# Kernel optimization log

Measured on AMD Instinct MI355X. Metric: run time of the kernel, lower is better.

The kernel has to match this reference:

```python
import jax, jax.numpy as jnp
import numpy as np

B, H, S, Q = 32768, 896, 448, 256  # batch, hidden, split=hidden//2, quantisation


def setup_inputs() -> dict:
    key = jax.random.key(0)
    ks = jax.random.split(key, 16)
    sc = 0.02
    return {
        'prev_y': jax.random.uniform(ks[0], (B, 2), jnp.float32) * 2.0 - 1.0,
        'prev_hidden': jax.random.normal(ks[1], (B, H), jnp.float32),
        'current_coarse': jax.random.uniform(ks[2], (B, 1), jnp.float32) * 2.0 - 1.0,
        'W_R': jax.random.normal(ks[3], (H, 3 * H), jnp.float32) * sc,
        'W_Ic': jax.random.normal(ks[4], (2, 3 * S), jnp.float32) * sc,
        'W_If': jax.random.normal(ks[5], (3, 3 * S), jnp.float32) * sc,
        'W_O1': jax.random.normal(ks[6], (S, S), jnp.float32) * sc,
        'b_O1': jnp.zeros((S,), jnp.float32),
        'W_O2': jax.random.normal(ks[7], (S, Q), jnp.float32) * sc,
        'b_O2': jnp.zeros((Q,), jnp.float32),
        'W_O3': jax.random.normal(ks[8], (S, S), jnp.float32) * sc,
        'b_O3': jnp.zeros((S,), jnp.float32),
        'W_O4': jax.random.normal(ks[9], (S, Q), jnp.float32) * sc,
        'b_O4': jnp.zeros((Q,), jnp.float32),
        'bias_u': jnp.zeros((H,), jnp.float32),
        'bias_r': jnp.zeros((H,), jnp.float32),
        'bias_e': jnp.zeros((H,), jnp.float32),
    }


def reference(prev_y, prev_hidden, current_coarse, W_R, W_Ic, W_If,
              W_O1, b_O1, W_O2, b_O2, W_O3, b_O3, W_O4, b_O4,
              bias_u, bias_r, bias_e):
    # recurrent projection of previous hidden state: [B, 3H]
    R_u, R_r, R_e = jnp.split(prev_hidden @ W_R, 3, axis=1)
    # coarse-half input projection from (prev_coarse, prev_fine): [B, 3S]
    I_cu, I_cr, I_ce = jnp.split(prev_y @ W_Ic, 3, axis=1)
    # fine-half input projection from (prev_coarse, prev_fine, current_coarse): [B, 3S]
    fine_in = jnp.concatenate([prev_y, current_coarse], axis=1)
    I_fu, I_fr, I_fe = jnp.split(fine_in @ W_If, 3, axis=1)
    I_u = jnp.concatenate([I_cu, I_fu], axis=1)
    I_r = jnp.concatenate([I_cr, I_fr], axis=1)
    I_e = jnp.concatenate([I_ce, I_fe], axis=1)
    u = jax.nn.sigmoid(R_u + I_u + bias_u)
    r = jax.nn.sigmoid(R_r + I_r + bias_r)
    e = jnp.tanh(r * R_e + I_e + bias_e)
    hidden = u * prev_hidden + (1.0 - u) * e
    h_c, h_f = jnp.split(hidden, 2, axis=1)
    out_coarse = jax.nn.relu(h_c @ W_O1 + b_O1) @ W_O2 + b_O2
    out_fine = jax.nn.relu(h_f @ W_O3 + b_O3) @ W_O4 + b_O4
    return out_coarse, out_fine, hidden
```

## Files before the change

kernel.cpp:

```cpp
#include <hip/hip_runtime.h>


typedef unsigned short u16;
typedef unsigned int u32;
typedef __attribute__((ext_vector_type(8))) short bf16x8;
typedef __attribute__((ext_vector_type(4))) float f32x4;

#define GAS __attribute__((address_space(1)))
#define LAS __attribute__((address_space(3)))

__device__ __forceinline__ u16 f2b(float f) {
  union { float f; u32 i; } v; v.f = f;
  return (u16)((v.i + 0x7fffu + ((v.i >> 16) & 1u)) >> 16);
}

__device__ __forceinline__ void gl_lds(const u16* g, u16* l) {
  __builtin_amdgcn_global_load_lds((const GAS void*)g, (LAS void*)l, 16, 0, 0);
}

__global__ void cvt_f32_bf16(const float* __restrict__ in, u16* __restrict__ outp) {
  const size_t i = ((size_t)blockIdx.x * 256 + threadIdx.x) * 4;
  const float4 v = *(const float4*)&in[i];
  ushort4 o;
  o.x = f2b(v.x); o.y = f2b(v.y); o.z = f2b(v.z); o.w = f2b(v.w);
  *(ushort4*)&outp[i] = o;
}

__global__ void transpose_f32_bf16(const float* __restrict__ in, u16* __restrict__ outp,
                                   int R, int C) {
  __shared__ u16 t[32][33];
  const int c0 = blockIdx.x * 32, r0 = blockIdx.y * 32;
  const int x = threadIdx.x, y = threadIdx.y;
  #pragma unroll
  for (int i = 0; i < 32; i += 8)
    t[y + i][x] = f2b(in[(size_t)(r0 + y + i) * C + (c0 + x)]);
  __syncthreads();
  #pragma unroll
  for (int i = 0; i < 32; i += 8)
    outp[(size_t)(c0 + y + i) * R + (r0 + x)] = t[x][y + i];
}

__device__ __forceinline__ void gemm_tile_k(const u16* __restrict__ A, int lda,
                                            const u16* __restrict__ BT, int ldb,
                                            int K, u16* Al, u16* Bl,
                                            int wave, int lane, f32x4 (&acc)[4][4]) {
  const int wm = wave & 1, wn = wave >> 1;
  const int q = lane >> 4, l16 = lane & 15;
  const int sr = lane >> 2;
  const int sc = (lane & 3) * 8;
  for (int k0 = 0; k0 < K; k0 += 32) {
    #pragma unroll
    for (int i = 0; i < 2; ++i) {
      const int rr = wave * 32 + i * 16;
      gl_lds(A + (size_t)(rr + sr) * lda + (k0 + sc), &Al[rr * 32]);
      gl_lds(BT + (size_t)(rr + sr) * ldb + (k0 + sc), &Bl[rr * 32]);
    }
    __syncthreads();
    bf16x8 af[4], bfr[4];
    #pragma unroll
    for (int t = 0; t < 4; ++t) {
      af[t]  = *(const bf16x8*)&Al[(wm * 64 + t * 16 + l16) * 32 + q * 8];
      bfr[t] = *(const bf16x8*)&Bl[(wn * 64 + t * 16 + l16) * 32 + q * 8];
    }
    #pragma unroll
    for (int mt = 0; mt < 4; ++mt)
      #pragma unroll
      for (int nt = 0; nt < 4; ++nt)
        acc[mt][nt] = __builtin_amdgcn_mfma_f32_16x16x32_bf16(af[mt], bfr[nt],
                                                              acc[mt][nt], 0, 0, 0);
    __syncthreads();
  }
}

__device__ __forceinline__ void zero_acc(f32x4 (&acc)[4][4]) {
  const f32x4 z = {0.f, 0.f, 0.f, 0.f};
  #pragma unroll
  for (int mt = 0; mt < 4; ++mt)
    #pragma unroll
    for (int nt = 0; nt < 4; ++nt)
      acc[mt][nt] = z;
}

__global__ __launch_bounds__(256, 2)
void gate_kernel(const u16* __restrict__ phb, const u16* __restrict__ wrt,
                 const float* __restrict__ phf,
                 const float* __restrict__ y2, const float* __restrict__ cc,
                 const float* __restrict__ wic, const float* __restrict__ wif,
                 const float* __restrict__ bu, const float* __restrict__ br,
                 const float* __restrict__ be,
                 float* __restrict__ houtf, u16* __restrict__ hb) {
  __shared__ u16 Al[128 * 32];
  __shared__ u16 Bl[3][128 * 32];
  __shared__ float rowy[3 * 128];
  const int tid = threadIdx.x;
  const int lane = tid & 63, wave = tid >> 6;
  const int f = blockIdx.x;
  const int xcd = f & 7, l = f >> 3;
  const int m0 = (xcd * 32 + l / 7) * 128;
  const int j0 = (l % 7) * 128;
  if (tid < 128) {
    const int r = m0 + tid;
    rowy[tid]       = y2[2 * r];
    rowy[128 + tid] = y2[2 * r + 1];
    rowy[256 + tid] = cc[r];
  }
  const int wm = wave & 1, wn = wave >> 1;
  const int q = lane >> 4, l16 = lane & 15;
  const int sr = lane >> 2, sc = (lane & 3) * 8;

  f32x4 acc[3][4][4];
  {
    const f32x4 z = {0.f, 0.f, 0.f, 0.f};
    #pragma unroll
    for (int s = 0; s < 3; ++s)
      #pragma unroll
      for (int mt = 0; mt < 4; ++mt)
        #pragma unroll
        for (int nt = 0; nt < 4; ++nt)
          acc[s][mt][nt] = z;
  }

  const u16* Ab  = phb + (size_t)m0 * 896;
  const u16* Bb0 = wrt + (size_t)(0 * 896 + j0) * 896;
  const u16* Bb1 = wrt + (size_t)(1 * 896 + j0) * 896;
  const u16* Bb2 = wrt + (size_t)(2 * 896 + j0) * 896;

  for (int k0 = 0; k0 < 896; k0 += 32) {
    #pragma unroll
    for (int i = 0; i < 2; ++i) {
      const int rr = wave * 32 + i * 16;
      const size_t go = (size_t)(rr + sr) * 896 + (k0 + sc);
      gl_lds(Ab  + go, &Al[rr * 32]);
      gl_lds(Bb0 + go, &Bl[0][rr * 32]);
      gl_lds(Bb1 + go, &Bl[1][rr * 32]);
      gl_lds(Bb2 + go, &Bl[2][rr * 32]);
    }
    __syncthreads();
    bf16x8 af[4];
    #pragma unroll
    for (int t = 0; t < 4; ++t)
      af[t] = *(const bf16x8*)&Al[(wm * 64 + t * 16 + l16) * 32 + q * 8];
    #pragma unroll
    for (int s = 0; s < 3; ++s) {
      bf16x8 bfr[4];
      #pragma unroll
      for (int t = 0; t < 4; ++t)
        bfr[t] = *(const bf16x8*)&Bl[s][(wn * 64 + t * 16 + l16) * 32 + q * 8];
      #pragma unroll
      for (int mt = 0; mt < 4; ++mt)
        #pragma unroll
        for (int nt = 0; nt < 4; ++nt)
          acc[s][mt][nt] = __builtin_amdgcn_mfma_f32_16x16x32_bf16(af[mt], bfr[nt],
                                                                   acc[s][mt][nt], 0, 0, 0);
    }
    __syncthreads();
  }

  const int jb = j0 + wn * 64;
  const int rb = wm * 64 + q * 4;
  #pragma unroll
  for (int nt = 0; nt < 4; ++nt) {
    const int j = jb + nt * 16 + l16;
    float wu0, wu1, wu2, wr0, wr1, wr2, we0, we1, we2;
    if (j < 448) {
      wu0 = wic[j];       wu1 = wic[1344 + j];       wu2 = 0.f;
      wr0 = wic[448 + j]; wr1 = wic[1792 + j];       wr2 = 0.f;
      we0 = wic[896 + j]; we1 = wic[2240 + j];       we2 = 0.f;
    } else {
      const int jf = j - 448;
      wu0 = wif[jf];       wu1 = wif[1344 + jf]; wu2 = wif[2688 + jf];
      wr0 = wif[448 + jf]; wr1 = wif[1792 + jf]; wr2 = wif[3136 + jf];
      we0 = wif[896 + jf]; we1 = wif[2240 + jf]; we2 = wif[3584 + jf];
    }
    const float bju = bu[j], bjr = br[j], bje = be[j];
    #pragma unroll
    for (int mt = 0; mt < 4; ++mt) {
      const int rl = rb + mt * 16;
      #pragma unroll
      for (int i = 0; i < 4; ++i) {
        const float y0 = rowy[rl + i], y1 = rowy[128 + rl + i], yc = rowy[256 + rl + i];
        const float gu = acc[0][mt][nt][i] + y0 * wu0 + y1 * wu1 + yc * wu2 + bju;
        const float gr = acc[1][mt][nt][i] + y0 * wr0 + y1 * wr1 + yc * wr2 + bjr;
        const float uu = 1.f / (1.f + __expf(-gu));
        const float rg = 1.f / (1.f + __expf(-gr));
        const float ev = tanhf(rg * acc[2][mt][nt][i] +
                               y0 * we0 + y1 * we1 + yc * we2 + bje);
        const size_t grow = (size_t)(m0 + rl + i);
        const float phv = phf[grow * 896 + j];
        const float h = uu * phv + (1.f - uu) * ev;
        houtf[grow * 896 + j] = h;
        hb[grow * 896 + j] = f2b(h);
      }
    }
  }
}

__global__ __launch_bounds__(256, 2)
void stage1_kernel(const u16* __restrict__ hb, const u16* __restrict__ w1t,
                   const u16* __restrict__ w3t, const float* __restrict__ b1,
                   const float* __restrict__ b3, u16* __restrict__ tc,
                   u16* __restrict__ tf) {
  __shared__ u16 Al[128 * 32];
  __shared__ u16 Bl[128 * 32];
  const int tid = threadIdx.x, lane = tid & 63, wave = tid >> 6;
  const int f = blockIdx.x;
  const int xcd = f & 7, l = f >> 3;
  const int mz = xcd * 64 + (l >> 2);
  const int z = mz >> 8;
  const int m0 = (mz & 255) * 128, n0 = (l & 3) * 128;
  const u16* A = hb + (size_t)m0 * 896 + z * 448;
  const u16* BT = (z ? w3t : w1t) + (size_t)n0 * 448;
  const float* bias = z ? b3 : b1;
  u16* T = z ? tf : tc;
  const int wm = wave & 1, wn = wave >> 1, q = lane >> 4, l16 = lane & 15;
  f32x4 acc[4][4];
  zero_acc(acc);
  gemm_tile_k(A, 896, BT, 448, 448, Al, Bl, wave, lane, acc);
  #pragma unroll
  for (int nt = 0; nt < 4; ++nt) {
    const int j = n0 + wn * 64 + nt * 16 + l16;
    if (j < 448) {
      const float bv = bias[j];
      #pragma unroll
      for (int mt = 0; mt < 4; ++mt)
        #pragma unroll
        for (int i = 0; i < 4; ++i) {
          const size_t row = (size_t)(m0 + wm * 64 + mt * 16 + q * 4 + i);
          T[row * 448 + j] = f2b(fmaxf(acc[mt][nt][i] + bv, 0.f));
        }
    }
  }
}

__global__ __launch_bounds__(256, 2)
void stage2_kernel(const u16* __restrict__ tc, const u16* __restrict__ tf,
                   const u16* __restrict__ w2t, const u16* __restrict__ w4t,
                   const float* __restrict__ b2_, const float* __restrict__ b4,
                   float* __restrict__ out) {
  __shared__ u16 Al[128 * 32];
  __shared__ u16 Bl[128 * 32];
  const int tid = threadIdx.x, lane = tid & 63, wave = tid >> 6;
  const int f = blockIdx.x;
  const int xcd = f & 7, l = f >> 3;
  const int mz = xcd * 64 + (l >> 1);
  const int z = mz >> 8;
  const int m0 = (mz & 255) * 128, n0 = (l & 1) * 128;
  const u16* A = (z ? tf : tc) + (size_t)m0 * 448;
  const u16* BT = (z ? w4t : w2t) + (size_t)n0 * 448;
  const float* bias = z ? b4 : b2_;
  float* O = out + (size_t)z * 32768 * 256;
  const int wm = wave & 1, wn = wave >> 1, q = lane >> 4, l16 = lane & 15;
  f32x4 acc[4][4];
  zero_acc(acc);
  gemm_tile_k(A, 448, BT, 448, 448, Al, Bl, wave, lane, acc);
  #pragma unroll
  for (int nt = 0; nt < 4; ++nt) {
    const int j = n0 + wn * 64 + nt * 16 + l16;
    const float bv = bias[j];
    #pragma unroll
    for (int mt = 0; mt < 4; ++mt)
      #pragma unroll
      for (int i = 0; i < 4; ++i) {
        const size_t row = (size_t)(m0 + wm * 64 + mt * 16 + q * 4 + i);
        O[row * 256 + j] = acc[mt][nt][i] + bv;
      }
  }
}

extern "C" void kernel_launch(void* const* d_in, const int* in_sizes, int n_in,
                              void* d_out, int out_size, void* d_ws, size_t ws_size,
                              hipStream_t stream) {
  const float* y2   = (const float*)d_in[0];
  const float* ph   = (const float*)d_in[1];
  const float* cc   = (const float*)d_in[2];
  const float* W_R  = (const float*)d_in[3];
  const float* W_Ic = (const float*)d_in[4];
  const float* W_If = (const float*)d_in[5];
  const float* W_O1 = (const float*)d_in[6];
  const float* b_O1 = (const float*)d_in[7];
  const float* W_O2 = (const float*)d_in[8];
  const float* b_O2 = (const float*)d_in[9];
  const float* W_O3 = (const float*)d_in[10];
  const float* b_O3 = (const float*)d_in[11];
  const float* W_O4 = (const float*)d_in[12];
  const float* b_O4 = (const float*)d_in[13];
  const float* bu   = (const float*)d_in[14];
  const float* br   = (const float*)d_in[15];
  const float* be   = (const float*)d_in[16];
  float* out = (float*)d_out;
  u16* ws  = (u16*)d_ws;

  u16* WRT = ws;
  u16* W1T = WRT + (size_t)2688 * 896;
  u16* W2T = W1T + 448 * 448;
  u16* W3T = W2T + 256 * 448;
  u16* W4T = W3T + 448 * 448;
  u16* phb = W4T + 256 * 448;
  u16* hb  = phb + (size_t)32768 * 896;
  u16* Tc  = phb;
  u16* Tf  = phb + (size_t)32768 * 448;
  float* hidf = out + (size_t)2 * 32768 * 256;

  dim3 tb(32, 8);
  cvt_f32_bf16<<<28672, 256, 0, stream>>>(ph, phb);
  transpose_f32_bf16<<<dim3(2688 / 32, 896 / 32), tb, 0, stream>>>(W_R, WRT, 896, 2688);
  transpose_f32_bf16<<<dim3(448 / 32, 448 / 32), tb, 0, stream>>>(W_O1, W1T, 448, 448);
  transpose_f32_bf16<<<dim3(256 / 32, 448 / 32), tb, 0, stream>>>(W_O2, W2T, 448, 256);
  transpose_f32_bf16<<<dim3(448 / 32, 448 / 32), tb, 0, stream>>>(W_O3, W3T, 448, 448);
  transpose_f32_bf16<<<dim3(256 / 32, 448 / 32), tb, 0, stream>>>(W_O4, W4T, 448, 256);

  gate_kernel<<<1792, 256, 0, stream>>>(phb, WRT, ph, y2, cc, W_Ic, W_If,
                                        bu, br, be, hidf, hb);
  stage1_kernel<<<2048, 256, 0, stream>>>(hb, W1T, W3T, b_O1, b_O3, Tc, Tf);
  stage2_kernel<<<1024, 256, 0, stream>>>(Tc, Tf, W2T, W4T, b_O2, b_O4, out);
}
```

Before: 707.9 us.

## Double-buffer LDS tiles in GEMM kernels and merge output-weight transposes

Adds double-buffered shared-memory staging to the gate, stage1 and stage2 GEMM loops. The global-to-LDS loads for the next K-step are issued before the MFMA work on the current step, so load latency can overlap compute and one barrier per step is removed. Separately, the four output-weight transpose launches are merged into one launch indexed by blockIdx.z, cutting launch overhead. The gate kernel's LDS use doubles (about 64KB per block), which may lower occupancy below the two blocks per CU that launch_bounds asks for.

```diff
diff --git a/kernel.cpp b/kernel.cpp
--- a/kernel.cpp
+++ b/kernel.cpp
@@ -26,10 +26,10 @@
   *(ushort4*)&outp[i] = o;
 }
 
-__global__ void transpose_f32_bf16(const float* __restrict__ in, u16* __restrict__ outp,
-                                   int R, int C) {
+__device__ __forceinline__ void transpose_body(const float* __restrict__ in,
+                                               u16* __restrict__ outp,
+                                               int R, int C, int c0, int r0) {
   __shared__ u16 t[32][33];
-  const int c0 = blockIdx.x * 32, r0 = blockIdx.y * 32;
   const int x = threadIdx.x, y = threadIdx.y;
   #pragma unroll
   for (int i = 0; i < 32; i += 8)
@@ -40,27 +40,57 @@
     outp[(size_t)(c0 + y + i) * R + (r0 + x)] = t[x][y + i];
 }
 
-__device__ __forceinline__ void gemm_tile_k(const u16* __restrict__ A, int lda,
-                                            const u16* __restrict__ BT, int ldb,
-                                            int K, u16* Al, u16* Bl,
-                                            int wave, int lane, f32x4 (&acc)[4][4]) {
+__global__ void transpose_f32_bf16(const float* __restrict__ in, u16* __restrict__ outp,
+                                   int R, int C) {
+  transpose_body(in, outp, R, C, blockIdx.x * 32, blockIdx.y * 32);
+}
+
+__global__ void transpose_wo(const float* __restrict__ w1, const float* __restrict__ w2,
+                             const float* __restrict__ w3, const float* __restrict__ w4,
+                             u16* __restrict__ o1, u16* __restrict__ o2,
+                             u16* __restrict__ o3, u16* __restrict__ o4) {
+  const int z = blockIdx.z;
+  const float* in = (z == 0) ? w1 : (z == 1) ? w2 : (z == 2) ? w3 : w4;
+  u16* outp = (z == 0) ? o1 : (z == 1) ? o2 : (z == 2) ? o3 : o4;
+  const int C = (z & 1) ? 256 : 448;
+  const int c0 = blockIdx.x * 32;
+  if (c0 >= C) return;
+  transpose_body(in, outp, 448, C, c0, blockIdx.y * 32);
+}
+
+__device__ __forceinline__ void gemm_tile_k_db(const u16* __restrict__ A, int lda,
+                                               const u16* __restrict__ BT, int ldb,
+                                               int K, u16 (&Al)[2][128 * 32],
+                                               u16 (&Bl)[2][128 * 32],
+                                               int wave, int lane, f32x4 (&acc)[4][4]) {
   const int wm = wave & 1, wn = wave >> 1;
   const int q = lane >> 4, l16 = lane & 15;
   const int sr = lane >> 2;
   const int sc = (lane & 3) * 8;
-  for (int k0 = 0; k0 < K; k0 += 32) {
-    #pragma unroll
-    for (int i = 0; i < 2; ++i) {
-      const int rr = wave * 32 + i * 16;
-      gl_lds(A + (size_t)(rr + sr) * lda + (k0 + sc), &Al[rr * 32]);
-      gl_lds(BT + (size_t)(rr + sr) * ldb + (k0 + sc), &Bl[rr * 32]);
-    }
-    __syncthreads();
+  const int nsteps = K / 32;
+  #pragma unroll
+  for (int i = 0; i < 2; ++i) {
+    const int rr = wave * 32 + i * 16;
+    gl_lds(A + (size_t)(rr + sr) * lda + sc, &Al[0][rr * 32]);
+    gl_lds(BT + (size_t)(rr + sr) * ldb + sc, &Bl[0][rr * 32]);
+  }
+  __syncthreads();
+  for (int t = 0; t < nsteps; ++t) {
+    const int cur = t & 1;
+    if (t + 1 < nsteps) {
+      const int k0 = (t + 1) * 32;
+      #pragma unroll
+      for (int i = 0; i < 2; ++i) {
+        const int rr = wave * 32 + i * 16;
+        gl_lds(A + (size_t)(rr + sr) * lda + (k0 + sc), &Al[cur ^ 1][rr * 32]);
+        gl_lds(BT + (size_t)(rr + sr) * ldb + (k0 + sc), &Bl[cur ^ 1][rr * 32]);
+      }
+    }
     bf16x8 af[4], bfr[4];
     #pragma unroll
-    for (int t = 0; t < 4; ++t) {
-      af[t]  = *(const bf16x8*)&Al[(wm * 64 + t * 16 + l16) * 32 + q * 8];
-      bfr[t] = *(const bf16x8*)&Bl[(wn * 64 + t * 16 + l16) * 32 + q * 8];
+    for (int t4 = 0; t4 < 4; ++t4) {
+      af[t4]  = *(const bf16x8*)&Al[cur][(wm * 64 + t4 * 16 + l16) * 32 + q * 8];
+      bfr[t4] = *(const bf16x8*)&Bl[cur][(wn * 64 + t4 * 16 + l16) * 32 + q * 8];
     }
     #pragma unroll
     for (int mt = 0; mt < 4; ++mt)
@@ -89,8 +119,8 @@
                  const float* __restrict__ bu, const float* __restrict__ br,
                  const float* __restrict__ be,
                  float* __restrict__ houtf, u16* __restrict__ hb) {
-  __shared__ u16 Al[128 * 32];
-  __shared__ u16 Bl[3][128 * 32];
+  __shared__ u16 Al[2][128 * 32];
+  __shared__ u16 Bl[2][3][128 * 32];
   __shared__ float rowy[3 * 128];
   const int tid = threadIdx.x;
   const int lane = tid & 63, wave = tid >> 6;
@@ -125,27 +155,41 @@
   const u16* Bb1 = wrt + (size_t)(1 * 896 + j0) * 896;
   const u16* Bb2 = wrt + (size_t)(2 * 896 + j0) * 896;
 
-  for (int k0 = 0; k0 < 896; k0 += 32) {
-    #pragma unroll
-    for (int i = 0; i < 2; ++i) {
-      const int rr = wave * 32 + i * 16;
-      const size_t go = (size_t)(rr + sr) * 896 + (k0 + sc);
-      gl_lds(Ab  + go, &Al[rr * 32]);
-      gl_lds(Bb0 + go, &Bl[0][rr * 32]);
-      gl_lds(Bb1 + go, &Bl[1][rr * 32]);
-      gl_lds(Bb2 + go, &Bl[2][rr * 32]);
-    }
-    __syncthreads();
+  #pragma unroll
+  for (int i = 0; i < 2; ++i) {
+    const int rr = wave * 32 + i * 16;
+    const size_t go = (size_t)(rr + sr) * 896 + sc;
+    gl_lds(Ab  + go, &Al[0][rr * 32]);
+    gl_lds(Bb0 + go, &Bl[0][0][rr * 32]);
+    gl_lds(Bb1 + go, &Bl[0][1][rr * 32]);
+    gl_lds(Bb2 + go, &Bl[0][2][rr * 32]);
+  }
+  __syncthreads();
+
+  for (int t = 0; t < 28; ++t) {
+    const int cur = t & 1;
+    if (t < 27) {
+      const int k0 = (t + 1) * 32;
+      #pragma unroll
+      for (int i = 0; i < 2; ++i) {
+        const int rr = wave * 32 + i * 16;
+        const size_t go = (size_t)(rr + sr) * 896 + (k0 + sc);
+        gl_lds(Ab  + go, &Al[cur ^ 1][rr * 32]);
+        gl_lds(Bb0 + go, &Bl[cur ^ 1][0][rr * 32]);
+        gl_lds(Bb1 + go, &Bl[cur ^ 1][1][rr * 32]);
+        gl_lds(Bb2 + go, &Bl[cur ^ 1][2][rr * 32]);
+      }
+    }
     bf16x8 af[4];
     #pragma unroll
-    for (int t = 0; t < 4; ++t)
-      af[t] = *(const bf16x8*)&Al[(wm * 64 + t * 16 + l16) * 32 + q * 8];
+    for (int t4 = 0; t4 < 4; ++t4)
+      af[t4] = *(const bf16x8*)&Al[cur][(wm * 64 + t4 * 16 + l16) * 32 + q * 8];
     #pragma unroll
     for (int s = 0; s < 3; ++s) {
       bf16x8 bfr[4];
       #pragma unroll
-      for (int t = 0; t < 4; ++t)
-        bfr[t] = *(const bf16x8*)&Bl[s][(wn * 64 + t * 16 + l16) * 32 + q * 8];
+      for (int t4 = 0; t4 < 4; ++t4)
+        bfr[t4] = *(const bf16x8*)&Bl[cur][s][(wn * 64 + t4 * 16 + l16) * 32 + q * 8];
       #pragma unroll
       for (int mt = 0; mt < 4; ++mt)
         #pragma unroll
@@ -200,8 +244,8 @@
                    const u16* __restrict__ w3t, const float* __restrict__ b1,
                    const float* __restrict__ b3, u16* __restrict__ tc,
                    u16* __restrict__ tf) {
-  __shared__ u16 Al[128 * 32];
-  __shared__ u16 Bl[128 * 32];
+  __shared__ u16 Al[2][128 * 32];
+  __shared__ u16 Bl[2][128 * 32];
   const int tid = threadIdx.x, lane = tid & 63, wave = tid >> 6;
   const int f = blockIdx.x;
   const int xcd = f & 7, l = f >> 3;
@@ -215,7 +259,7 @@
   const int wm = wave & 1, wn = wave >> 1, q = lane >> 4, l16 = lane & 15;
   f32x4 acc[4][4];
   zero_acc(acc);
-  gemm_tile_k(A, 896, BT, 448, 448, Al, Bl, wave, lane, acc);
+  gemm_tile_k_db(A, 896, BT, 448, 448, Al, Bl, wave, lane, acc);
   #pragma unroll
   for (int nt = 0; nt < 4; ++nt) {
     const int j = n0 + wn * 64 + nt * 16 + l16;
@@ -237,8 +281,8 @@
                    const u16* __restrict__ w2t, const u16* __restrict__ w4t,
                    const float* __restrict__ b2_, const float* __restrict__ b4,
                    float* __restrict__ out) {
-  __shared__ u16 Al[128 * 32];
-  __shared__ u16 Bl[128 * 32];
+  __shared__ u16 Al[2][128 * 32];
+  __shared__ u16 Bl[2][128 * 32];
   const int tid = threadIdx.x, lane = tid & 63, wave = tid >> 6;
   const int f = blockIdx.x;
   const int xcd = f & 7, l = f >> 3;
@@ -252,7 +296,7 @@
   const int wm = wave & 1, wn = wave >> 1, q = lane >> 4, l16 = lane & 15;
   f32x4 acc[4][4];
   zero_acc(acc);
-  gemm_tile_k(A, 448, BT, 448, 448, Al, Bl, wave, lane, acc);
+  gemm_tile_k_db(A, 448, BT, 448, 448, Al, Bl, wave, lane, acc);
   #pragma unroll
   for (int nt = 0; nt < 4; ++nt) {
     const int j = n0 + wn * 64 + nt * 16 + l16;
@@ -304,10 +348,8 @@
   dim3 tb(32, 8);
   cvt_f32_bf16<<<28672, 256, 0, stream>>>(ph, phb);
   transpose_f32_bf16<<<dim3(2688 / 32, 896 / 32), tb, 0, stream>>>(W_R, WRT, 896, 2688);
-  transpose_f32_bf16<<<dim3(448 / 32, 448 / 32), tb, 0, stream>>>(W_O1, W1T, 448, 448);
-  transpose_f32_bf16<<<dim3(256 / 32, 448 / 32), tb, 0, stream>>>(W_O2, W2T, 448, 256);
-  transpose_f32_bf16<<<dim3(448 / 32, 448 / 32), tb, 0, stream>>>(W_O3, W3T, 448, 448);
-  transpose_f32_bf16<<<dim3(256 / 32, 448 / 32), tb, 0, stream>>>(W_O4, W4T, 448, 256);
+  transpose_wo<<<dim3(14, 14, 4), tb, 0, stream>>>(W_O1, W_O2, W_O3, W_O4,
+                                                   W1T, W2T, W3T, W4T);
 
   gate_kernel<<<1792, 256, 0, stream>>>(phb, WRT, ph, y2, cc, W_Ic, W_If,
                                         bu, br, be, hidf, hb);
```

Result: no change. 703.4 us (-0.6%).

## Pipeline gate GEMM with triple-buffered LDS and 1024-thread blocks; merge weight transposes

Applied to the files above, without the earlier changes.

The gate kernel moves to 1024-thread blocks (16 waves), each wave owning a smaller 32x32 tile across the three gates. Global-to-LDS loads go into a three-stage ring buffer, with manual vmcnt waits and a single barrier per K step, so the loads for step t+2 overlap the MFMAs for step t. The tile-to-XCD mapping is also reordered. The four output-weight transposes are merged into one launch to save launch overhead. Risks are lower occupancy per CU (one 1024-thread block plus 96KB of LDS) and correctness depending on the hand-counted waitcnts.

```diff
diff --git a/kernel.cpp b/kernel.cpp
--- a/kernel.cpp
+++ b/kernel.cpp
@@ -26,10 +26,10 @@
   *(ushort4*)&outp[i] = o;
 }
 
-__global__ void transpose_f32_bf16(const float* __restrict__ in, u16* __restrict__ outp,
-                                   int R, int C) {
+__device__ __forceinline__ void transpose_body(const float* __restrict__ in,
+                                               u16* __restrict__ outp,
+                                               int R, int C, int c0, int r0) {
   __shared__ u16 t[32][33];
-  const int c0 = blockIdx.x * 32, r0 = blockIdx.y * 32;
   const int x = threadIdx.x, y = threadIdx.y;
   #pragma unroll
   for (int i = 0; i < 32; i += 8)
@@ -38,6 +38,24 @@
   #pragma unroll
   for (int i = 0; i < 32; i += 8)
     outp[(size_t)(c0 + y + i) * R + (r0 + x)] = t[x][y + i];
+}
+
+__global__ void transpose_f32_bf16(const float* __restrict__ in, u16* __restrict__ outp,
+                                   int R, int C) {
+  transpose_body(in, outp, R, C, blockIdx.x * 32, blockIdx.y * 32);
+}
+
+__global__ void transpose_wo(const float* __restrict__ w1, const float* __restrict__ w2,
+                             const float* __restrict__ w3, const float* __restrict__ w4,
+                             u16* __restrict__ o1, u16* __restrict__ o2,
+                             u16* __restrict__ o3, u16* __restrict__ o4) {
+  const int z = blockIdx.z;
+  const float* in = (z == 0) ? w1 : (z == 1) ? w2 : (z == 2) ? w3 : w4;
+  u16* outp = (z == 0) ? o1 : (z == 1) ? o2 : (z == 2) ? o3 : o4;
+  const int C = (z & 1) ? 256 : 448;
+  const int c0 = blockIdx.x * 32;
+  if (c0 >= C) return;
+  transpose_body(in, outp, 448, C, c0, blockIdx.y * 32);
 }
 
 __device__ __forceinline__ void gemm_tile_k(const u16* __restrict__ A, int lda,
@@ -81,7 +99,7 @@
       acc[mt][nt] = z;
 }
 
-__global__ __launch_bounds__(256, 2)
+__global__ __launch_bounds__(1024, 4)
 void gate_kernel(const u16* __restrict__ phb, const u16* __restrict__ wrt,
                  const float* __restrict__ phf,
                  const float* __restrict__ y2, const float* __restrict__ cc,
@@ -89,78 +107,84 @@
                  const float* __restrict__ bu, const float* __restrict__ br,
                  const float* __restrict__ be,
                  float* __restrict__ houtf, u16* __restrict__ hb) {
-  __shared__ u16 Al[128 * 32];
-  __shared__ u16 Bl[3][128 * 32];
+  __shared__ u16 Sl[3][16384];
   __shared__ float rowy[3 * 128];
   const int tid = threadIdx.x;
   const int lane = tid & 63, wave = tid >> 6;
   const int f = blockIdx.x;
   const int xcd = f & 7, l = f >> 3;
-  const int m0 = (xcd * 32 + l / 7) * 128;
-  const int j0 = (l % 7) * 128;
+  const int m0 = (xcd * 32 + (l & 31)) * 128;
+  const int j0 = (l >> 5) * 128;
   if (tid < 128) {
     const int r = m0 + tid;
     rowy[tid]       = y2[2 * r];
     rowy[128 + tid] = y2[2 * r + 1];
     rowy[256 + tid] = cc[r];
-  }
-  const int wm = wave & 1, wn = wave >> 1;
+    asm volatile("s_waitcnt lgkmcnt(0)" ::: "memory");
+  }
+  const int wm = wave & 3, wn = wave >> 2;
   const int q = lane >> 4, l16 = lane & 15;
   const int sr = lane >> 2, sc = (lane & 3) * 8;
 
-  f32x4 acc[3][4][4];
+  const int u0 = 2 * wave, u1 = u0 + 1;
+  const u16* g0; const u16* g1; int lo0, lo1;
+  if (u0 < 8) { g0 = phb + (size_t)(m0 + u0 * 16 + sr) * 896 + sc; lo0 = u0 * 512; }
+  else { const int nn = u0 - 8, jj = nn / 3, s = nn % 3;
+         g0 = wrt + (size_t)(s * 896 + j0 + jj * 16 + sr) * 896 + sc;
+         lo0 = 4096 + nn * 512; }
+  if (u1 < 8) { g1 = phb + (size_t)(m0 + u1 * 16 + sr) * 896 + sc; lo1 = u1 * 512; }
+  else { const int nn = u1 - 8, jj = nn / 3, s = nn % 3;
+         g1 = wrt + (size_t)(s * 896 + j0 + jj * 16 + sr) * 896 + sc;
+         lo1 = 4096 + nn * 512; }
+
+  f32x4 acc[2][3][2];
   {
     const f32x4 z = {0.f, 0.f, 0.f, 0.f};
     #pragma unroll
-    for (int s = 0; s < 3; ++s)
-      #pragma unroll
-      for (int mt = 0; mt < 4; ++mt)
+    for (int a = 0; a < 2; ++a)
+      #pragma unroll
+      for (int s = 0; s < 3; ++s)
         #pragma unroll
-        for (int nt = 0; nt < 4; ++nt)
-          acc[s][mt][nt] = z;
-  }
-
-  const u16* Ab  = phb + (size_t)m0 * 896;
-  const u16* Bb0 = wrt + (size_t)(0 * 896 + j0) * 896;
-  const u16* Bb1 = wrt + (size_t)(1 * 896 + j0) * 896;
-  const u16* Bb2 = wrt + (size_t)(2 * 896 + j0) * 896;
-
-  for (int k0 = 0; k0 < 896; k0 += 32) {
-    #pragma unroll
-    for (int i = 0; i < 2; ++i) {
-      const int rr = wave * 32 + i * 16;
-      const size_t go = (size_t)(rr + sr) * 896 + (k0 + sc);
-      gl_lds(Ab  + go, &Al[rr * 32]);
-      gl_lds(Bb0 + go, &Bl[0][rr * 32]);
-      gl_lds(Bb1 + go, &Bl[1][rr * 32]);
-      gl_lds(Bb2 + go, &Bl[2][rr * 32]);
-    }
-    __syncthreads();
-    bf16x8 af[4];
-    #pragma unroll
-    for (int t = 0; t < 4; ++t)
-      af[t] = *(const bf16x8*)&Al[(wm * 64 + t * 16 + l16) * 32 + q * 8];
-    #pragma unroll
-    for (int s = 0; s < 3; ++s) {
-      bf16x8 bfr[4];
-      #pragma unroll
-      for (int t = 0; t < 4; ++t)
-        bfr[t] = *(const bf16x8*)&Bl[s][(wn * 64 + t * 16 + l16) * 32 + q * 8];
-      #pragma unroll
-      for (int mt = 0; mt < 4; ++mt)
+        for (int m = 0; m < 2; ++m)
+          acc[a][s][m] = z;
+  }
+
+  auto stage = [&](int t_) {
+    const int b_ = t_ % 3;
+    const int k_ = t_ * 32;
+    gl_lds(g0 + k_, &Sl[b_][lo0]);
+    gl_lds(g1 + k_, &Sl[b_][lo1]);
+  };
+
+  stage(0);
+  stage(1);
+  for (int t = 0; t < 28; ++t) {
+    if (t < 27) asm volatile("s_waitcnt vmcnt(2)" ::: "memory");
+    else        asm volatile("s_waitcnt vmcnt(0)" ::: "memory");
+    __builtin_amdgcn_s_barrier();
+    __builtin_amdgcn_sched_barrier(0);
+    const u16* Sb = Sl[t % 3];
+    bf16x8 af[2];
+    #pragma unroll
+    for (int mt = 0; mt < 2; ++mt)
+      af[mt] = *(const bf16x8*)&Sb[(wm * 32 + mt * 16 + l16) * 32 + q * 8];
+    #pragma unroll
+    for (int jj2 = 0; jj2 < 2; ++jj2)
+      #pragma unroll
+      for (int s = 0; s < 3; ++s) {
+        const int nn = (2 * wn + jj2) * 3 + s;
+        const bf16x8 bf_ = *(const bf16x8*)&Sb[4096 + nn * 512 + l16 * 32 + q * 8];
         #pragma unroll
-        for (int nt = 0; nt < 4; ++nt)
-          acc[s][mt][nt] = __builtin_amdgcn_mfma_f32_16x16x32_bf16(af[mt], bfr[nt],
-                                                                   acc[s][mt][nt], 0, 0, 0);
-    }
-    __syncthreads();
-  }
-
-  const int jb = j0 + wn * 64;
-  const int rb = wm * 64 + q * 4;
-  #pragma unroll
-  for (int nt = 0; nt < 4; ++nt) {
-    const int j = jb + nt * 16 + l16;
+        for (int mt = 0; mt < 2; ++mt)
+          acc[jj2][s][mt] = __builtin_amdgcn_mfma_f32_16x16x32_bf16(
+              af[mt], bf_, acc[jj2][s][mt], 0, 0, 0);
+      }
+    if (t + 2 < 28) stage(t + 2);
+  }
+
+  #pragma unroll
+  for (int jj2 = 0; jj2 < 2; ++jj2) {
+    const int j = j0 + (2 * wn + jj2) * 16 + l16;
     float wu0, wu1, wu2, wr0, wr1, wr2, we0, we1, we2;
     if (j < 448) {
       wu0 = wic[j];       wu1 = wic[1344 + j];       wu2 = 0.f;
@@ -174,16 +198,16 @@
     }
     const float bju = bu[j], bjr = br[j], bje = be[j];
     #pragma unroll
-    for (int mt = 0; mt < 4; ++mt) {
-      const int rl = rb + mt * 16;
+    for (int mt = 0; mt < 2; ++mt) {
+      const int rl = wm * 32 + mt * 16 + q * 4;
       #pragma unroll
       for (int i = 0; i < 4; ++i) {
         const float y0 = rowy[rl + i], y1 = rowy[128 + rl + i], yc = rowy[256 + rl + i];
-        const float gu = acc[0][mt][nt][i] + y0 * wu0 + y1 * wu1 + yc * wu2 + bju;
-        const float gr = acc[1][mt][nt][i] + y0 * wr0 + y1 * wr1 + yc * wr2 + bjr;
+        const float gu = acc[jj2][0][mt][i] + y0 * wu0 + y1 * wu1 + yc * wu2 + bju;
+        const float gr = acc[jj2][1][mt][i] + y0 * wr0 + y1 * wr1 + yc * wr2 + bjr;
         const float uu = 1.f / (1.f + __expf(-gu));
         const float rg = 1.f / (1.f + __expf(-gr));
-        const float ev = tanhf(rg * acc[2][mt][nt][i] +
+        const float ev = tanhf(rg * acc[jj2][2][mt][i] +
                                y0 * we0 + y1 * we1 + yc * we2 + bje);
         const size_t grow = (size_t)(m0 + rl + i);
         const float phv = phf[grow * 896 + j];
@@ -304,13 +328,11 @@
   dim3 tb(32, 8);
   cvt_f32_bf16<<<28672, 256, 0, stream>>>(ph, phb);
   transpose_f32_bf16<<<dim3(2688 / 32, 896 / 32), tb, 0, stream>>>(W_R, WRT, 896, 2688);
-  transpose_f32_bf16<<<dim3(448 / 32, 448 / 32), tb, 0, stream>>>(W_O1, W1T, 448, 448);
-  transpose_f32_bf16<<<dim3(256 / 32, 448 / 32), tb, 0, stream>>>(W_O2, W2T, 448, 256);
-  transpose_f32_bf16<<<dim3(448 / 32, 448 / 32), tb, 0, stream>>>(W_O3, W3T, 448, 448);
-  transpose_f32_bf16<<<dim3(256 / 32, 448 / 32), tb, 0, stream>>>(W_O4, W4T, 448, 256);
-
-  gate_kernel<<<1792, 256, 0, stream>>>(phb, WRT, ph, y2, cc, W_Ic, W_If,
-                                        bu, br, be, hidf, hb);
+  transpose_wo<<<dim3(14, 14, 4), tb, 0, stream>>>(W_O1, W_O2, W_O3, W_O4,
+                                                   W1T, W2T, W3T, W4T);
+
+  gate_kernel<<<1792, 1024, 0, stream>>>(phb, WRT, ph, y2, cc, W_Ic, W_If,
+                                         bu, br, be, hidf, hb);
   stage1_kernel<<<2048, 256, 0, stream>>>(hb, W1T, W3T, b_O1, b_O3, Tc, Tf);
   stage2_kernel<<<1024, 256, 0, stream>>>(Tc, Tf, W2T, W4T, b_O2, b_O4, out);
 }
```

Result: faster. 628.9 us (-11.2%).
